# Optimization experiments

Measured on AMD Instinct MI355X. Metric: run time of the kernel, lower is better.

The kernel has to match this reference:

```python
import jax, jax.numpy as jnp
import numpy as np

B, N, ESM_DIM, D, K = 256, 100000, 1280, 512, 8
ATT_TAU = 1.0
NEG_INF_FILL = -10000.0
EPS = 1e-6


def _l2norm(x, axis=-1):
    return x / jnp.linalg.norm(x, axis=axis, keepdims=True).clip(1e-12)


def setup_inputs() -> dict:
    key = jax.random.key(0)
    ks = jax.random.split(key, 8)
    index_emb = _l2norm(jax.random.normal(ks[0], (N, ESM_DIM), jnp.float32))
    return {
        "query_esm_pooled": jax.random.normal(ks[1], (B, ESM_DIM), jnp.float32),
        "model_embs": jax.random.normal(ks[2], (B, D), jnp.float32),
        "index_emb": index_emb,
        "index_labels": jax.random.randint(ks[3], (N,), 0, 2, jnp.int64),
        "exclude_idx": jax.random.randint(ks[4], (B,), 0, N, jnp.int64),
        "proj_W": jax.random.normal(ks[5], (ESM_DIM, D), jnp.float32) * 0.02,
        "proj_b": jnp.zeros((D,), jnp.float32),
        "clf_W": jax.random.normal(ks[6], (2 * D, 2), jnp.float32) * 0.02,
        "clf_b": jnp.zeros((2,), jnp.float32),
    }


def reference(query_esm_pooled, model_embs, index_emb, index_labels, exclude_idx,
              proj_W, proj_b, clf_W, clf_b):
    # esm_dim != model_emb_dim -> use ESM-pooled queries, project neighbors
    Q = _l2norm(query_esm_pooled)                       # [B, E]
    sims = Q @ index_emb.T                              # [B, N] cosine (index pre-normalized)
    sims = sims.at[jnp.arange(B), exclude_idx].set(NEG_INF_FILL)
    _, topk = jax.lax.top_k(sims, K)                    # [B, K]

    neigh_raw = index_emb[topk]                         # [B, K, E]
    neigh_lbl = index_labels[topk]                      # [B, K]
    neigh_proj = neigh_raw @ proj_W + proj_b            # [B, K, D]

    # tiny cross-attention: query = model_embs, keys/values = neighbors
    scale = 1.0 / (jnp.sqrt(jnp.float32(D)) * ATT_TAU)
    att = jax.nn.softmax(jnp.einsum('bd,bkd->bk', model_embs, neigh_proj) * scale, axis=-1)
    z_neigh = jnp.einsum('bk,bkd->bd', att, neigh_proj)  # [B, D]

    logits_retr = jnp.concatenate([model_embs, z_neigh], axis=1) @ clf_W + clf_b  # [B, 2]

    # prototypes (detached, matching torch.no_grad)
    mask_pos = (neigh_lbl == 1).astype(jnp.float32)     # [B, K]
    mask_neg = (neigh_lbl == 0).astype(jnp.float32)
    pos_proto = jnp.einsum('bk,bkd->bd', mask_pos, neigh_proj) / (mask_pos.sum(1, keepdims=True) + EPS)
    neg_proto = jnp.einsum('bk,bkd->bd', mask_neg, neigh_proj) / (mask_neg.sum(1, keepdims=True) + EPS)
    pos_proto = jax.lax.stop_gradient(pos_proto)
    neg_proto = jax.lax.stop_gradient(neg_proto)

    retr_align_loss = jnp.mean((model_embs - pos_proto) ** 2) - 0.5 * jnp.mean((model_embs - neg_proto) ** 2)
    return logits_retr, retr_align_loss
```

## Files before the change

### kernel.cpp

```cpp
#include <hip/hip_runtime.h>
#include <hip/hip_bf16.h>
#include <math.h>

#define B_SZ 256
#define N_SZ 100000
#define E_SZ 1280
#define D_SZ 512

#define NCH 1563

typedef __attribute__((ext_vector_type(8))) short s8v;
typedef __attribute__((ext_vector_type(4))) float f32x4;

__device__ __forceinline__ unsigned short f2bf(float f) {
  unsigned int u = __float_as_uint(f);
  u += 0x7fffu + ((u >> 16) & 1u);
  return (unsigned short)(u >> 16);
}
__device__ __forceinline__ unsigned int pack2(float a, float b) {
  union { __hip_bfloat162 h; unsigned u; } c;
  c.h = __float22bfloat162_rn(make_float2(a, b));
  return c.u;
}
__device__ __forceinline__ void gload16(const void* g, void* l) {
  __builtin_amdgcn_global_load_lds(
      (const __attribute__((address_space(1))) void*)g,
      (__attribute__((address_space(3))) void*)l, 16, 0, 0);
}

#define TOP8_UPDATE(v_, i_)                                                 \
  if ((v_) > minv) {                                                        \
    _Pragma("unroll")                                                       \
    for (int s_ = 0; s_ < 8; ++s_)                                          \
      if (s_ == mins) { bv[s_] = (v_); bi[s_] = (i_); }                     \
    minv = bv[0]; mins = 0;                                                 \
    _Pragma("unroll")                                                       \
    for (int s_ = 1; s_ < 8; ++s_)                                          \
      if (bv[s_] < minv) { minv = bv[s_]; mins = s_; }                      \
  }

__global__ __launch_bounds__(256) void k_conv(const float* __restrict__ in,
                                              unsigned short* __restrict__ outp) {
  const size_t T = (size_t)gridDim.x * 256;
  const size_t total = 16000000u;
  for (size_t i = (size_t)blockIdx.x * 256 + threadIdx.x; i < total; i += T) {
    const float4* p = ((const float4*)in) + 2 * i;
    float4 a = p[0], b = p[1];
    uint4 o;
    o.x = pack2(a.x, a.y); o.y = pack2(a.z, a.w);
    o.z = pack2(b.x, b.y); o.w = pack2(b.z, b.w);
    ((uint4*)outp)[i] = o;
  }
}

__global__ __launch_bounds__(256) void k_prep(const float* __restrict__ q,
                                              unsigned short* __restrict__ qn,
                                              const float* __restrict__ W,
                                              unsigned short* __restrict__ Wt) {
  __shared__ __align__(16) char sm[64 * 65 * 4];
  const int t = threadIdx.x;
  if (blockIdx.x < 256) {
    float* red = (float*)sm;
    int row = blockIdx.x;
    const float* src = q + (size_t)row * E_SZ;
    float x[5];
    float ss = 0.f;
#pragma unroll
    for (int i = 0; i < 5; ++i) { x[i] = src[t + 256 * i]; ss += x[i] * x[i]; }
#pragma unroll
    for (int o = 32; o > 0; o >>= 1) ss += __shfl_down(ss, o, 64);
    if ((t & 63) == 0) red[t >> 6] = ss;
    __syncthreads();
    float nrm = sqrtf(red[0] + red[1] + red[2] + red[3]);
    nrm = fmaxf(nrm, 1e-12f);
    float inv = 1.0f / nrm;
    unsigned short* dst = qn + (size_t)row * E_SZ;
#pragma unroll
    for (int i = 0; i < 5; ++i) dst[t + 256 * i] = f2bf(x[i] * inv);
  } else {
    float (*T)[65] = (float(*)[65])sm;
    int idx = blockIdx.x - 256;
    int kb = (idx % 20) * 64;
    int nb = (idx / 20) * 64;
#pragma unroll
    for (int i = 0; i < 16; ++i) {
      int kr = i * 4 + (t >> 6);
      T[kr][t & 63] = W[(size_t)(kb + kr) * D_SZ + nb + (t & 63)];
    }
    __syncthreads();
    const int n = t >> 2, ks = (t & 3) * 16;
    unsigned int ow[8];
#pragma unroll
    for (int j = 0; j < 8; ++j)
      ow[j] = (unsigned)f2bf(T[ks + 2 * j][n]) |
              ((unsigned)f2bf(T[ks + 2 * j + 1][n]) << 16);
    unsigned short* dst = Wt + (size_t)(nb + n) * E_SZ + kb + ks;
    *(uint4*)dst = make_uint4(ow[0], ow[1], ow[2], ow[3]);
    *(uint4*)(dst + 8) = make_uint4(ow[4], ow[5], ow[6], ow[7]);
  }
}

__global__ __launch_bounds__(256) void k_sims_topk(
    const unsigned short* __restrict__ qn, const unsigned short* __restrict__ ebf,
    const int* __restrict__ excl, float* __restrict__ cval) {
  __shared__ __align__(16) char lds[61440];
  const int t = threadIdx.x;
  const int l = t & 63, w = t >> 6;
  const int r15 = l & 15, g = l >> 4;
  const int jbase = blockIdx.x * 64;
  const int myq = (w << 6) + l;
  const int ex = excl[myq];

  f32x4 acc[4][4];
#pragma unroll
  for (int i = 0; i < 4; ++i)
#pragma unroll
    for (int j = 0; j < 4; ++j) acc[i][j] = (f32x4)0.f;

  int afoff[4], bfoff[4];
#pragma unroll
  for (int mq = 0; mq < 4; ++mq)
    afoff[mq] = ((w << 6) + 16 * mq + r15) * 64 + g * 16;
#pragma unroll
  for (int nj = 0; nj < 4; ++nj)
    bfoff[nj] = (16 * nj + r15) * 64 + g * 16;

  const int srow = t >> 2, skc = (t & 3) * 8;
  const unsigned short* aS0 = qn + (size_t)(srow) * E_SZ + skc;
  const unsigned short* aS1 = qn + (size_t)(64 + srow) * E_SZ + skc;
  const unsigned short* aS2 = qn + (size_t)(128 + srow) * E_SZ + skc;
  const unsigned short* aS3 = qn + (size_t)(192 + srow) * E_SZ + skc;
  const unsigned short* bS =
      ebf + (size_t)min(jbase + srow, N_SZ - 1) * E_SZ + skc;
  const int adst = t * 16;

#define STAGE(kt_, ab_, bb_)                                                 \
  { gload16(aS0 + (kt_), lds + (ab_) + adst);                                \
    gload16(aS1 + (kt_), lds + (ab_) + 4096 + adst);                         \
    gload16(aS2 + (kt_), lds + (ab_) + 8192 + adst);                         \
    gload16(aS3 + (kt_), lds + (ab_) + 12288 + adst);                        \
    gload16(bS + (kt_), lds + (bb_) + adst); }

  STAGE(0, 0, 49152);
  STAGE(32, 16384, 53248);

  int ab0 = 0, ab1 = 16384, ab2 = 32768;
  int bb0 = 49152, bb1 = 53248, bb2 = 57344;

  for (int s = 0; s < 40; ++s) {
    if (s < 39) {
      asm volatile("s_waitcnt vmcnt(5)" ::: "memory");
    } else {
      asm volatile("s_waitcnt vmcnt(0)" ::: "memory");
    }
    __builtin_amdgcn_s_barrier();
    {
      s8v af[4], bf[4];
#pragma unroll
      for (int mq = 0; mq < 4; ++mq)
        af[mq] = *(const s8v*)(lds + ab0 + afoff[mq]);
#pragma unroll
      for (int nj = 0; nj < 4; ++nj)
        bf[nj] = *(const s8v*)(lds + bb0 + bfoff[nj]);
#pragma unroll
      for (int nj = 0; nj < 4; ++nj)
#pragma unroll
        for (int mq = 0; mq < 4; ++mq)
          acc[mq][nj] = __builtin_amdgcn_mfma_f32_16x16x32_bf16(
              af[mq], bf[nj], acc[mq][nj], 0, 0, 0);
    }
    asm volatile("s_waitcnt lgkmcnt(0)" ::: "memory");
    __builtin_amdgcn_s_barrier();
    if (s + 2 < 40) STAGE((s + 2) * 32, ab2, bb2);
    int ta = ab0; ab0 = ab1; ab1 = ab2; ab2 = ta;
    int tb = bb0; bb0 = bb1; bb1 = bb2; bb2 = tb;
  }
#undef STAGE

  for (int ph = 0; ph < 2; ++ph) {
    if ((w >> 1) == ph) {
      float* Sbuf = (float*)(lds + (w & 1) * 16640);
#pragma unroll
      for (int mq = 0; mq < 4; ++mq)
#pragma unroll
        for (int nj = 0; nj < 4; ++nj)
#pragma unroll
          for (int r = 0; r < 4; ++r)
            Sbuf[(16 * mq + 4 * g + r) * 65 + 16 * nj + r15] = acc[mq][nj][r];
      float bv[8]; int bi[8];
#pragma unroll
      for (int s = 0; s < 8; ++s) { bv[s] = -1e30f; bi[s] = 0; }
      float minv = -1e30f; int mins = 0;
      const float* Srow = Sbuf + l * 65;
      for (int c = 0; c < 64; ++c) {
        int gj = jbase + c;
        float v = Srow[c];
        if (gj < N_SZ && gj != ex) { TOP8_UPDATE(v, gj); }
      }
      float* vdst = cval + (size_t)blockIdx.x * 4096 + myq * 8;
      *(float4*)vdst = make_float4(bv[0], bv[1], bv[2], bv[3]);
      *(float4*)(vdst + 4) = make_float4(bv[4], bv[5], bv[6], bv[7]);
      int* idst = (int*)(cval + (size_t)blockIdx.x * 4096 + 2048) + myq * 8;
      *(int4*)idst = make_int4(bi[0], bi[1], bi[2], bi[3]);
      *(int4*)(idst + 4) = make_int4(bi[4], bi[5], bi[6], bi[7]);
    }
    __syncthreads();
  }
}

__global__ __launch_bounds__(256) void k_merge(const float* __restrict__ cval,
                                               int* __restrict__ topk) {
  __shared__ float sv[2048];
  __shared__ int si[2048];
  const int q = blockIdx.x, t = threadIdx.x;
  float bv[8]; int bi[8];
#pragma unroll
  for (int s = 0; s < 8; ++s) { bv[s] = -1e30f; bi[s] = 0; }
  float minv = -1e30f; int mins = 0;
  for (int c = t; c < NCH; c += 256) {
    const float* vp = cval + (size_t)c * 4096 + q * 8;
    const int* ip = (const int*)(cval + (size_t)c * 4096 + 2048) + q * 8;
    float4 v0 = *(const float4*)vp, v1 = *(const float4*)(vp + 4);
    int4 i0 = *(const int4*)ip, i1 = *(const int4*)(ip + 4);
    float va[8] = {v0.x, v0.y, v0.z, v0.w, v1.x, v1.y, v1.z, v1.w};
    int ia[8] = {i0.x, i0.y, i0.z, i0.w, i1.x, i1.y, i1.z, i1.w};
#pragma unroll
    for (int s = 0; s < 8; ++s) {
      float v = va[s]; int ix = ia[s];
      TOP8_UPDATE(v, ix);
    }
  }
#pragma unroll
  for (int s = 0; s < 8; ++s) { sv[t * 8 + s] = bv[s]; si[t * 8 + s] = bi[s]; }
  __syncthreads();
  if (t < 64) {
    for (int rr = 1; rr < 4; ++rr) {
      int r = t + rr * 64;
#pragma unroll
      for (int s = 0; s < 8; ++s) {
        float v = sv[r * 8 + s]; int ix = si[r * 8 + s];
        TOP8_UPDATE(v, ix);
      }
    }
#pragma unroll
    for (int s = 0; s < 8; ++s) { sv[t * 8 + s] = bv[s]; si[t * 8 + s] = bi[s]; }
  }
  __syncthreads();
  if (t < 8) {
    for (int rr = 1; rr < 8; ++rr) {
      int r = t + rr * 8;
#pragma unroll
      for (int s = 0; s < 8; ++s) {
        float v = sv[r * 8 + s]; int ix = si[r * 8 + s];
        TOP8_UPDATE(v, ix);
      }
    }
#pragma unroll
    for (int s = 0; s < 8; ++s) { sv[t * 8 + s] = bv[s]; si[t * 8 + s] = bi[s]; }
  }
  __syncthreads();
  if (t == 0) {
    for (int r = 1; r < 8; ++r) {
#pragma unroll
      for (int s = 0; s < 8; ++s) {
        float v = sv[r * 8 + s]; int ix = si[r * 8 + s];
        TOP8_UPDATE(v, ix);
      }
    }
#pragma unroll
    for (int s = 0; s < 8; ++s) topk[q * 8 + s] = bi[s];
  }
}

__global__ __launch_bounds__(256) void k_proj(
    const float* __restrict__ emb, const int* __restrict__ topk,
    const unsigned short* __restrict__ Wt, const float* __restrict__ bias,
    float* __restrict__ nproj) {
  __shared__ __align__(16) char lds[65536];
  const int t = threadIdx.x, l = t & 63, w = t >> 6;
  const int r15 = l & 15, g = l >> 4;
  const int wm = w >> 1, wn = w & 1;
  const int r0 = blockIdx.x * 128, n0 = blockIdx.y * 128;
  const int sr = t >> 3, kc = t & 7;

  int grow[4];
#pragma unroll
  for (int i = 0; i < 4; ++i) grow[i] = topk[r0 + i * 32 + sr];

  int woff[4];
#pragma unroll
  for (int i = 0; i < 4; ++i) {
    int row = i * 32 + sr;
    woff[i] = row * 128 + (((kc + (row & 7)) & 7) << 4);
  }
  int afoff[2][4], bfoff[2][4];
#pragma unroll
  for (int h = 0; h < 2; ++h) {
#pragma unroll
    for (int qq = 0; qq < 4; ++qq) {
      int rowa = 64 * wm + 16 * qq + r15;
      afoff[h][qq] = rowa * 128 + ((((h << 2) + g + (rowa & 7)) & 7) << 4);
      int rowb = 64 * wn + 16 * qq + r15;
      bfoff[h][qq] = rowb * 128 + ((((h << 2) + g + (rowb & 7)) & 7) << 4);
    }
  }

  f32x4 acc[4][4];
#pragma unroll
  for (int i = 0; i < 4; ++i)
#pragma unroll
    for (int j = 0; j < 4; ++j) acc[i][j] = (f32x4)0.f;

  float4 aset[4][2];
  s8v bset[4];

#define PLOADA(kt_)                                                          \
  { _Pragma("unroll") for (int i_ = 0; i_ < 4; ++i_) {                       \
      const float* s_ = emb + (size_t)grow[i_] * E_SZ + (kt_) + kc * 8;      \
      aset[i_][0] = *(const float4*)s_;                                      \
      aset[i_][1] = *(const float4*)(s_ + 4); } }
#define PLOADB(kt_)                                                          \
  { _Pragma("unroll") for (int i_ = 0; i_ < 4; ++i_)                         \
      bset[i_] = *(const s8v*)(Wt + (size_t)(n0 + i_ * 32 + sr) * E_SZ +     \
                               (kt_) + kc * 8); }
#define PWR(bA_, bB_)                                                        \
  { _Pragma("unroll") for (int i_ = 0; i_ < 4; ++i_) {                       \
      uint4 p_;                                                              \
      p_.x = pack2(aset[i_][0].x, aset[i_][0].y);                            \
      p_.y = pack2(aset[i_][0].z, aset[i_][0].w);                            \
      p_.z = pack2(aset[i_][1].x, aset[i_][1].y);                            \
      p_.w = pack2(aset[i_][1].z, aset[i_][1].w);                            \
      *(uint4*)((bA_) + woff[i_]) = p_;                                      \
      *(s8v*)((bB_) + woff[i_]) = bset[i_]; } }
#define PCOMP(bA_, bB_)                                                      \
  { _Pragma("unroll") for (int h_ = 0; h_ < 2; ++h_) {                       \
      s8v af_[4], bf_[4];                                                    \
      _Pragma("unroll") for (int q_ = 0; q_ < 4; ++q_) {                     \
        af_[q_] = *(const s8v*)((bA_) + afoff[h_][q_]);                      \
        bf_[q_] = *(const s8v*)((bB_) + bfoff[h_][q_]); }                    \
      _Pragma("unroll") for (int nj_ = 0; nj_ < 4; ++nj_)                    \
        _Pragma("unroll") for (int mq_ = 0; mq_ < 4; ++mq_)                  \
          acc[mq_][nj_] = __builtin_amdgcn_mfma_f32_16x16x32_bf16(           \
              af_[mq_], bf_[nj_], acc[mq_][nj_], 0, 0, 0); } }

  PLOADA(0); PLOADB(0);
  PWR(lds, lds + 32768);
  __syncthreads();
  for (int s = 0; s < 20; ++s) {
    char* cA = lds + (s & 1) * 16384;
    char* cB = lds + 32768 + (s & 1) * 16384;
    char* nA = lds + ((s + 1) & 1) * 16384;
    char* nB = lds + 32768 + ((s + 1) & 1) * 16384;
    if (s + 1 < 20) { PLOADA((s + 1) * 64); PLOADB((s + 1) * 64); }
    PCOMP(cA, cB);
    if (s + 1 < 20) { PWR(nA, nB); }
    __syncthreads();
  }
#pragma unroll
  for (int nj = 0; nj < 4; ++nj) {
    int n = n0 + 64 * wn + 16 * nj + r15;
    float bn = bias[n];
#pragma unroll
    for (int mq = 0; mq < 4; ++mq) {
      int m = r0 + 64 * wm + 16 * mq + 4 * g;
#pragma unroll
      for (int r = 0; r < 4; ++r)
        nproj[(size_t)(m + r) * D_SZ + n] = acc[mq][nj][r] + bn;
    }
  }
#undef PLOADA
#undef PLOADB
#undef PWR
#undef PCOMP
}

__global__ __launch_bounds__(256) void k_attn(
    const float* __restrict__ model, const float* __restrict__ proj,
    const int* __restrict__ topk, const int* __restrict__ labels,
    const float* __restrict__ clfW, const float* __restrict__ clfb,
    float* __restrict__ out, float* __restrict__ lossp) {
  __shared__ float P[8 * 512];
  __shared__ float red[4];
  int b = blockIdx.x, t = threadIdx.x;
  const float* src = proj + (size_t)b * 8 * 512;
#pragma unroll
  for (int i = 0; i < 4; ++i) {
    int o = i * 1024 + t * 4;
    *(float4*)&P[o] = *(const float4*)&src[o];
  }
  __syncthreads();
  float m0 = model[b * 512 + t], m1 = model[b * 512 + 256 + t];

  float sc[8];
#pragma unroll
  for (int k = 0; k < 8; ++k) {
    float p = m0 * P[k * 512 + t] + m1 * P[k * 512 + 256 + t];
#pragma unroll
    for (int o = 32; o > 0; o >>= 1) p += __shfl_down(p, o, 64);
    if ((t & 63) == 0) red[t >> 6] = p;
    __syncthreads();
    sc[k] = red[0] + red[1] + red[2] + red[3];
    __syncthreads();
  }
  const float scale = 0.04419417382415922f;
  float mx = -1e30f;
  float s_[8];
#pragma unroll
  for (int k = 0; k < 8; ++k) { s_[k] = sc[k] * scale; mx = fmaxf(mx, s_[k]); }
  float den = 0.f, att[8];
#pragma unroll
  for (int k = 0; k < 8; ++k) { att[k] = expf(s_[k] - mx); den += att[k]; }
  float iden = 1.0f / den;
#pragma unroll
  for (int k = 0; k < 8; ++k) att[k] *= iden;

  float z0 = 0.f, z1 = 0.f;
#pragma unroll
  for (int k = 0; k < 8; ++k) {
    z0 = fmaf(att[k], P[k * 512 + t], z0);
    z1 = fmaf(att[k], P[k * 512 + 256 + t], z1);
  }
#pragma unroll
  for (int c = 0; c < 2; ++c) {
    float lp = m0 * clfW[t * 2 + c] + m1 * clfW[(t + 256) * 2 + c] +
               z0 * clfW[(512 + t) * 2 + c] + z1 * clfW[(768 + t) * 2 + c];
#pragma unroll
    for (int o = 32; o > 0; o >>= 1) lp += __shfl_down(lp, o, 64);
    if ((t & 63) == 0) red[t >> 6] = lp;
    __syncthreads();
    if (t == 0) out[b * 2 + c] = red[0] + red[1] + red[2] + red[3] + clfb[c];
    __syncthreads();
  }
  float cp = 0.f, cn = 0.f;
  float p0 = 0.f, p1 = 0.f, n0 = 0.f, n1 = 0.f;
#pragma unroll
  for (int k = 0; k < 8; ++k) {
    int lb = labels[topk[b * 8 + k]];
    float mp = (lb == 1) ? 1.f : 0.f;
    float mn = (lb == 0) ? 1.f : 0.f;
    cp += mp; cn += mn;
    p0 = fmaf(mp, P[k * 512 + t], p0);
    p1 = fmaf(mp, P[k * 512 + 256 + t], p1);
    n0 = fmaf(mn, P[k * 512 + t], n0);
    n1 = fmaf(mn, P[k * 512 + 256 + t], n1);
  }
  float icp = 1.0f / (cp + 1e-6f), icn = 1.0f / (cn + 1e-6f);
  p0 *= icp; p1 *= icp; n0 *= icn; n1 *= icn;
  float lq = (m0 - p0) * (m0 - p0) + (m1 - p1) * (m1 - p1) -
             0.5f * ((m0 - n0) * (m0 - n0) + (m1 - n1) * (m1 - n1));
#pragma unroll
  for (int o = 32; o > 0; o >>= 1) lq += __shfl_down(lq, o, 64);
  if ((t & 63) == 0) red[t >> 6] = lq;
  __syncthreads();
  if (t == 0) lossp[b] = red[0] + red[1] + red[2] + red[3];
}

__global__ __launch_bounds__(256) void k_loss(const float* __restrict__ lossp,
                                              float* __restrict__ out) {
  __shared__ float red[4];
  int t = threadIdx.x;
  float v = lossp[t];
#pragma unroll
  for (int o = 32; o > 0; o >>= 1) v += __shfl_down(v, o, 64);
  if ((t & 63) == 0) red[t >> 6] = v;
  __syncthreads();
  if (t == 0)
    out[512] = (red[0] + red[1] + red[2] + red[3]) * (1.0f / (256.0f * 512.0f));
}

extern "C" void kernel_launch(void* const* d_in, const int* in_sizes, int n_in,
                              void* d_out, int out_size, void* d_ws,
                              size_t ws_size, hipStream_t stream) {
  (void)in_sizes; (void)n_in; (void)out_size; (void)ws_size;
  const float* q      = (const float*)d_in[0];
  const float* model  = (const float*)d_in[1];
  const float* emb    = (const float*)d_in[2];
  const int*   labels = (const int*)d_in[3];
  const int*   excl   = (const int*)d_in[4];
  const float* projW  = (const float*)d_in[5];
  const float* projb  = (const float*)d_in[6];
  const float* clfW   = (const float*)d_in[7];
  const float* clfb   = (const float*)d_in[8];
  float* out = (float*)d_out;

  char* ws = (char*)d_ws;
  unsigned short* qn  = (unsigned short*)ws;
  unsigned short* Wt  = (unsigned short*)(ws + 655360);
  unsigned short* ebf = (unsigned short*)(ws + 1966080);
  float* cval  = (float*)(ws + 257966080);
  int*   topk  = (int*)(ws + 283574272);
  float* nproj = (float*)(ws + 283582464);
  float* lossp = (float*)(ws + 287776768);

  k_prep<<<416, 256, 0, stream>>>(q, qn, projW, Wt);
  k_conv<<<2048, 256, 0, stream>>>(emb, ebf);
  k_sims_topk<<<NCH, 256, 0, stream>>>(qn, ebf, excl, cval);
  k_merge<<<256, 256, 0, stream>>>(cval, topk);
  k_proj<<<dim3(16, 4), 256, 0, stream>>>(emb, topk, Wt, projb, nproj);
  k_attn<<<256, 256, 0, stream>>>(model, nproj, topk, labels, clfW, clfb, out, lossp);
  k_loss<<<1, 256, 0, stream>>>(lossp, out);
}
```

Measured before the change: 465.0 us.

## Fuse fp32-to-bf16 index conversion into the similarity GEMM loader

Removes the separate conversion kernel that wrote a bf16 copy of the 100000x1280 index embedding. The similarity kernel now loads fp32 rows into registers three stages ahead, converts them to bf16 and writes them into LDS itself, while the query tiles still use async global-to-LDS loads. This avoids writing and re-reading a 256 MB intermediate. In exchange it adds register pressure and a more complex pipeline with hand-tuned waitcnt values that must stay correct.

```diff
diff --git a/kernel.cpp b/kernel.cpp
--- a/kernel.cpp
+++ b/kernel.cpp
@@ -38,20 +38,6 @@
     for (int s_ = 1; s_ < 8; ++s_)                                          \
       if (bv[s_] < minv) { minv = bv[s_]; mins = s_; }                      \
   }
-
-__global__ __launch_bounds__(256) void k_conv(const float* __restrict__ in,
-                                              unsigned short* __restrict__ outp) {
-  const size_t T = (size_t)gridDim.x * 256;
-  const size_t total = 16000000u;
-  for (size_t i = (size_t)blockIdx.x * 256 + threadIdx.x; i < total; i += T) {
-    const float4* p = ((const float4*)in) + 2 * i;
-    float4 a = p[0], b = p[1];
-    uint4 o;
-    o.x = pack2(a.x, a.y); o.y = pack2(a.z, a.w);
-    o.z = pack2(b.x, b.y); o.w = pack2(b.z, b.w);
-    ((uint4*)outp)[i] = o;
-  }
-}
 
 __global__ __launch_bounds__(256) void k_prep(const float* __restrict__ q,
                                               unsigned short* __restrict__ qn,
@@ -101,7 +87,7 @@
 }
 
 __global__ __launch_bounds__(256) void k_sims_topk(
-    const unsigned short* __restrict__ qn, const unsigned short* __restrict__ ebf,
+    const unsigned short* __restrict__ qn, const float* __restrict__ emb,
     const int* __restrict__ excl, float* __restrict__ cval) {
   __shared__ __align__(16) char lds[61440];
   const int t = threadIdx.x;
@@ -130,52 +116,64 @@
   const unsigned short* aS1 = qn + (size_t)(64 + srow) * E_SZ + skc;
   const unsigned short* aS2 = qn + (size_t)(128 + srow) * E_SZ + skc;
   const unsigned short* aS3 = qn + (size_t)(192 + srow) * E_SZ + skc;
-  const unsigned short* bS =
-      ebf + (size_t)min(jbase + srow, N_SZ - 1) * E_SZ + skc;
   const int adst = t * 16;
 
-#define STAGE(kt_, ab_, bb_)                                                 \
+  const float* bS = emb + (size_t)min(jbase + srow, N_SZ - 1) * E_SZ + skc;
+  const int bwoff = srow * 64 + (t & 3) * 16;
+  float4 br[3][2];
+
+#define STAGEA(kt_, ab_)                                                     \
   { gload16(aS0 + (kt_), lds + (ab_) + adst);                                \
     gload16(aS1 + (kt_), lds + (ab_) + 4096 + adst);                         \
     gload16(aS2 + (kt_), lds + (ab_) + 8192 + adst);                         \
-    gload16(aS3 + (kt_), lds + (ab_) + 12288 + adst);                        \
-    gload16(bS + (kt_), lds + (bb_) + adst); }
-
-  STAGE(0, 0, 49152);
-  STAGE(32, 16384, 53248);
-
-  int ab0 = 0, ab1 = 16384, ab2 = 32768;
-  int bb0 = 49152, bb1 = 53248, bb2 = 57344;
+    gload16(aS3 + (kt_), lds + (ab_) + 12288 + adst); }
+#define LOADB(set_, kt_)                                                     \
+  { set_[0] = *(const float4*)(bS + (kt_));                                  \
+    set_[1] = *(const float4*)(bS + (kt_) + 4); }
+#define CVTWR(set_, bb_)                                                     \
+  { uint4 p_;                                                                \
+    p_.x = pack2(set_[0].x, set_[0].y); p_.y = pack2(set_[0].z, set_[0].w);  \
+    p_.z = pack2(set_[1].x, set_[1].y); p_.w = pack2(set_[1].z, set_[1].w);  \
+    *(uint4*)(lds + (bb_) + bwoff) = p_; }
+#define COMPUTE(ab_, bb_)                                                    \
+  { s8v af_[4], bf_[4];                                                      \
+    _Pragma("unroll") for (int mq_ = 0; mq_ < 4; ++mq_)                      \
+      af_[mq_] = *(const s8v*)(lds + (ab_) + afoff[mq_]);                    \
+    _Pragma("unroll") for (int nj_ = 0; nj_ < 4; ++nj_)                      \
+      bf_[nj_] = *(const s8v*)(lds + (bb_) + bfoff[nj_]);                    \
+    _Pragma("unroll") for (int nj_ = 0; nj_ < 4; ++nj_)                      \
+      _Pragma("unroll") for (int mq_ = 0; mq_ < 4; ++mq_)                    \
+        acc[mq_][nj_] = __builtin_amdgcn_mfma_f32_16x16x32_bf16(             \
+            af_[mq_], bf_[nj_], acc[mq_][nj_], 0, 0, 0); }
+
+  const int AB[3] = {0, 16384, 32768};
+  const int BB[3] = {49152, 53248, 57344};
+
+  LOADB(br[0], 0);
+  LOADB(br[1], 32);
+  LOADB(br[2], 64);
+  STAGEA(0, 0);
+  STAGEA(32, 16384);
+  CVTWR(br[0], 49152);
+  asm volatile("s_waitcnt vmcnt(4) lgkmcnt(0)" ::: "memory");
+  __builtin_amdgcn_s_barrier();
 
   for (int s = 0; s < 40; ++s) {
-    if (s < 39) {
-      asm volatile("s_waitcnt vmcnt(5)" ::: "memory");
+    if (s + 3 < 40) LOADB(br[s % 3], (s + 3) * 32);
+    if (s + 2 < 40) STAGEA((s + 2) * 32, AB[(s + 2) % 3]);
+    if (s + 1 < 40) CVTWR(br[(s + 1) % 3], BB[(s + 1) % 3]);
+    COMPUTE(AB[s % 3], BB[s % 3]);
+    if (s + 2 < 40) {
+      asm volatile("s_waitcnt vmcnt(6) lgkmcnt(0)" ::: "memory");
     } else {
-      asm volatile("s_waitcnt vmcnt(0)" ::: "memory");
+      asm volatile("s_waitcnt vmcnt(0) lgkmcnt(0)" ::: "memory");
     }
     __builtin_amdgcn_s_barrier();
-    {
-      s8v af[4], bf[4];
-#pragma unroll
-      for (int mq = 0; mq < 4; ++mq)
-        af[mq] = *(const s8v*)(lds + ab0 + afoff[mq]);
-#pragma unroll
-      for (int nj = 0; nj < 4; ++nj)
-        bf[nj] = *(const s8v*)(lds + bb0 + bfoff[nj]);
-#pragma unroll
-      for (int nj = 0; nj < 4; ++nj)
-#pragma unroll
-        for (int mq = 0; mq < 4; ++mq)
-          acc[mq][nj] = __builtin_amdgcn_mfma_f32_16x16x32_bf16(
-              af[mq], bf[nj], acc[mq][nj], 0, 0, 0);
-    }
-    asm volatile("s_waitcnt lgkmcnt(0)" ::: "memory");
-    __builtin_amdgcn_s_barrier();
-    if (s + 2 < 40) STAGE((s + 2) * 32, ab2, bb2);
-    int ta = ab0; ab0 = ab1; ab1 = ab2; ab2 = ta;
-    int tb = bb0; bb0 = bb1; bb1 = bb2; bb2 = tb;
-  }
-#undef STAGE
+  }
+#undef STAGEA
+#undef LOADB
+#undef CVTWR
+#undef COMPUTE
 
   for (int ph = 0; ph < 2; ++ph) {
     if ((w >> 1) == ph) {
@@ -484,17 +482,15 @@
   float* out = (float*)d_out;
 
   char* ws = (char*)d_ws;
-  unsigned short* qn  = (unsigned short*)ws;
-  unsigned short* Wt  = (unsigned short*)(ws + 655360);
-  unsigned short* ebf = (unsigned short*)(ws + 1966080);
-  float* cval  = (float*)(ws + 257966080);
-  int*   topk  = (int*)(ws + 283574272);
-  float* nproj = (float*)(ws + 283582464);
-  float* lossp = (float*)(ws + 287776768);
+  unsigned short* qn = (unsigned short*)ws;
+  unsigned short* Wt = (unsigned short*)(ws + 655360);
+  float* cval  = (float*)(ws + 1966080);
+  int*   topk  = (int*)(ws + 27574272);
+  float* nproj = (float*)(ws + 27582464);
+  float* lossp = (float*)(ws + 31776768);
 
   k_prep<<<416, 256, 0, stream>>>(q, qn, projW, Wt);
-  k_conv<<<2048, 256, 0, stream>>>(emb, ebf);
-  k_sims_topk<<<NCH, 256, 0, stream>>>(qn, ebf, excl, cval);
+  k_sims_topk<<<NCH, 256, 0, stream>>>(qn, emb, excl, cval);
   k_merge<<<256, 256, 0, stream>>>(cval, topk);
   k_proj<<<dim3(16, 4), 256, 0, stream>>>(emb, topk, Wt, projb, nproj);
   k_attn<<<256, 256, 0, stream>>>(model, nproj, topk, labels, clfW, clfb, out, lossp);
```

After: 544.5 us. 1.17x slower.
